# Performance work log

Measured on AMD Instinct MI355X. Metric: run time of the kernel, lower is better.

## Reference

```python
import jax, jax.numpy as jnp
import numpy as np

H_DIM = 1152
N_HEADS = 12
HEAD_DIM = H_DIM // N_HEADS  # 96, divisible by 3
SCALE_ROT = 32 // 16  # character_pixel_size // patch_size


def setup_inputs() -> dict:
    key = jax.random.key(0)
    ks = jax.random.split(key, 9)
    std = 1.0 / np.sqrt(H_DIM)
    return {
        "hidden_states": jax.random.normal(ks[0], (8, 1025, H_DIM), dtype=jnp.float32),
        "Wq": jax.random.normal(ks[1], (H_DIM, H_DIM), dtype=jnp.float32) * std,
        "bq": jax.random.normal(ks[2], (H_DIM,), dtype=jnp.float32) * 0.02,
        "Wk": jax.random.normal(ks[3], (H_DIM, H_DIM), dtype=jnp.float32) * std,
        "bk": jax.random.normal(ks[4], (H_DIM,), dtype=jnp.float32) * 0.02,
        "Wv": jax.random.normal(ks[5], (H_DIM, H_DIM), dtype=jnp.float32) * std,
        "bv": jax.random.normal(ks[6], (H_DIM,), dtype=jnp.float32) * 0.02,
        "Wo": jax.random.normal(ks[7], (H_DIM, H_DIM), dtype=jnp.float32) * std,
        "bo": jax.random.normal(ks[8], (H_DIM,), dtype=jnp.float32) * 0.02,
        "rows": 32,
        "cols": 32,
    }


def _rotary_tables(seq_len, rows, cols, dtype):
    # (seq_len, n_triplets) trig tables based on 2-D patch grid position
    inv_freq = 1.0 / (10000.0 ** (jnp.arange(0, HEAD_DIM, 3, dtype=dtype) / (HEAD_DIM * SCALE_ROT)))
    ids = jnp.arange(seq_len)
    cls_offset = 1 if seq_len != rows * cols else 0
    grid_ids = jnp.clip(ids - cls_offset, 0)
    row_ids = (grid_ids // cols).astype(dtype)
    col_ids = (grid_ids % cols).astype(dtype)
    theta = row_ids[:, None] * inv_freq
    psi = col_ids[:, None] * inv_freq
    return jnp.cos(theta), jnp.sin(theta), jnp.cos(psi), jnp.sin(psi)


def _apply_rotary_3d(x, ct, st, cp, sp):
    # x: (b, s, h, d) -> view as (b, s, h, t, 3)
    b, s, h, d = x.shape
    x = x.reshape(b, s, h, d // 3, 3)
    ct = ct[None, :, None, :]
    st = st[None, :, None, :]
    cp = cp[None, :, None, :]
    sp = sp[None, :, None, :]
    x0, x1, x2 = x[..., 0], x[..., 1], x[..., 2]
    r0 = cp * x0 + sp * st * x1 + sp * ct * x2
    r1 = ct * x1 - st * x2
    r2 = -sp * x0 + cp * st * x1 + cp * ct * x2
    return jnp.stack((r0, r1, r2), axis=-1).reshape(b, s, h, d)


def reference(hidden_states, Wq, bq, Wk, bk, Wv, bv, Wo, bo, rows, cols):
    b, s, _ = hidden_states.shape
    dtype = hidden_states.dtype
    scale = HEAD_DIM ** -0.5

    q = (hidden_states @ Wq + bq).reshape(b, s, N_HEADS, HEAD_DIM)
    k = (hidden_states @ Wk + bk).reshape(b, s, N_HEADS, HEAD_DIM)
    v = (hidden_states @ Wv + bv).reshape(b, s, N_HEADS, HEAD_DIM)

    ct, st, cp, sp = _rotary_tables(s, rows, cols, dtype)
    q = _apply_rotary_3d(q, ct, st, cp, sp)
    k = _apply_rotary_3d(k, ct, st, cp, sp)

    # (b, h, s, s) attention scores
    scores = jnp.einsum("bqhd,bkhd->bhqk", q, k) * scale
    probs = jax.nn.softmax(scores.astype(jnp.float32), axis=-1).astype(dtype)
    ctx = jnp.einsum("bhqk,bkhd->bqhd", probs, v).reshape(b, s, H_DIM)
    out = ctx @ Wo + bo
    return out
```

## Files before the change

### kernel.cpp

```cpp
#include <hip/hip_runtime.h>
#include <stdint.h>

#define BATCH 8
#define SEQ   1025
#define HDIM  1152
#define NH    12
#define DH    96
#define MROWS (BATCH*SEQ)
#define N_QKV (3*HDIM)
#define KD    HDIM
#define NTK   36

typedef __attribute__((ext_vector_type(8))) short short8;
typedef __attribute__((ext_vector_type(4))) short short4_;
typedef __attribute__((ext_vector_type(4))) float float4_;
typedef __attribute__((ext_vector_type(16))) float f32x16;

#define AS1 __attribute__((address_space(1)))
#define AS3 __attribute__((address_space(3)))
#define BARM() do { asm volatile("" ::: "memory"); __builtin_amdgcn_s_barrier(); asm volatile("" ::: "memory"); } while (0)

__device__ inline float bf2f(short s) {
  union { unsigned u; float f; } x; x.u = ((unsigned)(unsigned short)s) << 16; return x.f;
}
__device__ inline short f2bf(float f) {
  union { float f; unsigned u; } x; x.f = f;
  unsigned r = (x.u + 0x7fffu + ((x.u >> 16) & 1u)) >> 16;
  return (short)r;
}

__global__ __launch_bounds__(256) void convx(const float* __restrict__ hs, short* __restrict__ X) {
  int i = blockIdx.x * 256 + threadIdx.x;
  float4_ v = ((const float4_*)hs)[i];
  short4_ o;
  o[0] = f2bf(v[0]); o[1] = f2bf(v[1]); o[2] = f2bf(v[2]); o[3] = f2bf(v[3]);
  ((short4_*)X)[i] = o;
}

__global__ __launch_bounds__(256) void convw_qkv(const float* __restrict__ Wq,
                                                 const float* __restrict__ Wk,
                                                 const float* __restrict__ Wv,
                                                 short* __restrict__ Wt) {
  long e = (long)blockIdx.x * 256 + threadIdx.x;
  int n = (int)(e / KD), k = (int)(e % KD);
  const float* W = n < HDIM ? Wq : (n < 2 * HDIM ? Wk : Wv);
  int nn = n < HDIM ? n : (n < 2 * HDIM ? n - HDIM : n - 2 * HDIM);
  Wt[e] = f2bf(W[(long)k * HDIM + nn]);
}

__global__ __launch_bounds__(256) void convw_o(const float* __restrict__ Wo, short* __restrict__ Wot) {
  long e = (long)blockIdx.x * 256 + threadIdx.x;
  int n = (int)(e / HDIM), k = (int)(e % HDIM);
  Wot[e] = f2bf(Wo[(long)k * HDIM + n]);
}

template<int OUTF32>
__global__ __launch_bounds__(512, 1) void gemm256(
    const short* __restrict__ A, const short* __restrict__ Bt,
    const float* __restrict__ b0, const float* __restrict__ b1, const float* __restrict__ b2,
    void* __restrict__ Cout, const int N, const int MT) {
  __shared__ alignas(16) short Lds[32768];
  const int tid = threadIdx.x;
  const int l = tid & 63, w = tid >> 6;
  const int col = l & 31, hi = l >> 5;
  const int wr = w >> 2, wc = w & 3;

  const int nwg = gridDim.x;
  const int qq = nwg >> 3, r8 = nwg & 7;
  const int xcd = blockIdx.x & 7, loc = blockIdx.x >> 3;
  const int wg = (xcd < r8 ? xcd * (qq + 1) : r8 * (qq + 1) + (xcd - r8) * qq) + loc;
  const int mt = wg % MT, nt = wg / MT;
  const int m0 = mt * 256, n0 = nt * 256;

  const int key = (tid >> 3) & 7;
  const short* asrc[2]; const short* bsrc[2];
#pragma unroll
  for (int i = 0; i < 2; ++i) {
    int g = (i * 512 + tid) ^ key;
    int rowl = g >> 2, colE = (g & 3) * 8;
    int ra = m0 + rowl; if (ra > MROWS - 1) ra = MROWS - 1;
    int rb = n0 + rowl; if (rb > N - 1) rb = N - 1;
    asrc[i] = A + (long)ra * KD + colE;
    bsrc[i] = Bt + (long)rb * KD + colE;
  }

#define STAGE_A(buf, kt_, i) \
  __builtin_amdgcn_global_load_lds((const AS1 void*)(asrc[i] + (kt_) * 32), \
      (AS3 void*)(&Lds[(buf) * 8192 + (i) * 4096 + tid * 8]), 16, 0, 0)
#define STAGE_B(buf, kt_, i) \
  __builtin_amdgcn_global_load_lds((const AS1 void*)(bsrc[i] + (kt_) * 32), \
      (AS3 void*)(&Lds[16384 + (buf) * 8192 + (i) * 4096 + tid * 8]), 16, 0, 0)

  const int keyx = ((col >> 1) & 7) << 3;
  const int fcol = hi * 8;
#define LDSA(buf, mi, ks) (*(const short8*)&Lds[(buf) * 8192 + \
    ((((wr * 128 + (mi) * 32 + col) << 5) + ((ks) << 4) + fcol) ^ keyx)])
#define LDSB(buf, nj, ks) (*(const short8*)&Lds[16384 + (buf) * 8192 + \
    ((((wc * 64 + (nj) * 32 + col) << 5) + ((ks) << 4) + fcol) ^ keyx)])
#define MFMA32(a, b, c) __builtin_amdgcn_mfma_f32_32x32x16_bf16(a, b, c, 0, 0, 0)

  f32x16 acc[4][2];
#pragma unroll
  for (int mi = 0; mi < 4; ++mi)
#pragma unroll
    for (int nj = 0; nj < 2; ++nj) acc[mi][nj] = (f32x16)(0.f);

  STAGE_A(0, 0, 0); STAGE_A(0, 0, 1);
  STAGE_B(0, 0, 0); STAGE_B(0, 0, 1);
  STAGE_B(1, 1, 0); STAGE_B(1, 1, 1);
  asm volatile("s_waitcnt vmcnt(2)" ::: "memory");
  BARM();

  for (int kt = 0; kt < NTK; ++kt) {
    const int cur = kt & 1, nxt = cur ^ 1;
    short8 b00 = LDSB(cur, 0, 0), b01 = LDSB(cur, 0, 1);
    short8 b10 = LDSB(cur, 1, 0), b11 = LDSB(cur, 1, 1);
    short8 a00 = LDSA(cur, 0, 0), a01 = LDSA(cur, 0, 1);
    short8 a10 = LDSA(cur, 1, 0), a11 = LDSA(cur, 1, 1);
    if (kt + 1 < NTK) { STAGE_A(nxt, kt + 1, 0); STAGE_A(nxt, kt + 1, 1); }
    BARM();
    __builtin_amdgcn_s_setprio(1);
    acc[0][0] = MFMA32(a00, b00, acc[0][0]);
    acc[0][1] = MFMA32(a00, b10, acc[0][1]);
    acc[1][0] = MFMA32(a10, b00, acc[1][0]);
    acc[1][1] = MFMA32(a10, b10, acc[1][1]);
    acc[0][0] = MFMA32(a01, b01, acc[0][0]);
    acc[0][1] = MFMA32(a01, b11, acc[0][1]);
    acc[1][0] = MFMA32(a11, b01, acc[1][0]);
    acc[1][1] = MFMA32(a11, b11, acc[1][1]);
    __builtin_amdgcn_s_setprio(0);
    BARM();
    short8 a20 = LDSA(cur, 2, 0), a21 = LDSA(cur, 2, 1);
    short8 a30 = LDSA(cur, 3, 0), a31 = LDSA(cur, 3, 1);
    if (kt + 2 < NTK) { STAGE_B(cur, kt + 2, 0); STAGE_B(cur, kt + 2, 1); }
    if (kt < NTK - 2) asm volatile("s_waitcnt vmcnt(2)" ::: "memory");
    else              asm volatile("s_waitcnt vmcnt(0)" ::: "memory");
    BARM();
    __builtin_amdgcn_s_setprio(1);
    acc[2][0] = MFMA32(a20, b00, acc[2][0]);
    acc[2][1] = MFMA32(a20, b10, acc[2][1]);
    acc[3][0] = MFMA32(a30, b00, acc[3][0]);
    acc[3][1] = MFMA32(a30, b10, acc[3][1]);
    acc[2][0] = MFMA32(a21, b01, acc[2][0]);
    acc[2][1] = MFMA32(a21, b11, acc[2][1]);
    acc[3][0] = MFMA32(a31, b01, acc[3][0]);
    acc[3][1] = MFMA32(a31, b11, acc[3][1]);
    __builtin_amdgcn_s_setprio(0);
    BARM();
  }

  float bias[2];
#pragma unroll
  for (int nj = 0; nj < 2; ++nj) {
    int cn = n0 + wc * 64 + nj * 32 + col;
    float bv_ = 0.f;
    if (cn < N) bv_ = (N == HDIM) ? b0[cn]
                                  : (cn < HDIM ? b0[cn] : (cn < 2 * HDIM ? b1[cn - HDIM] : b2[cn - 2 * HDIM]));
    bias[nj] = bv_;
  }
#pragma unroll
  for (int mi = 0; mi < 4; ++mi)
#pragma unroll
    for (int g = 0; g < 4; ++g)
#pragma unroll
      for (int t2 = 0; t2 < 4; ++t2) {
        int rowi = m0 + wr * 128 + mi * 32 + g * 8 + hi * 4 + t2;
        if (rowi >= MROWS) continue;
#pragma unroll
        for (int nj = 0; nj < 2; ++nj) {
          int cn = n0 + wc * 64 + nj * 32 + col;
          if (cn >= N) continue;
          float v = acc[mi][nj][g * 4 + t2] + bias[nj];
          if (OUTF32) ((float*)Cout)[(long)rowi * N + cn] = v;
          else        ((short*)Cout)[(long)rowi * N + cn] = f2bf(v);
        }
      }
#undef STAGE_A
#undef STAGE_B
#undef LDSA
#undef LDSB
#undef MFMA32
}

__global__ __launch_bounds__(256) void rotary_kernel(short* __restrict__ QKV,
                                                     const int* __restrict__ rowsp,
                                                     const int* __restrict__ colsp) {
  int idx = blockIdx.x * 256 + threadIdx.x;
  int j = idx & 31;
  int t = idx >> 5;
  int h = t % NH;
  int m = t / NH;
  int s = m % SEQ;
  int cols = colsp[0];
  int rws = rowsp[0];
  int off = (SEQ != rws * cols) ? 1 : 0;
  int gid = s - off; if (gid < 0) gid = 0;
  int row = gid / cols, col = gid % cols;
  float invf = exp2f((float)(3 * j) * (-13.287712379549449f / 192.0f));
  float th = row * invf, ps = col * invf;
  float st, ct, sp, cp;
  __sincosf(th, &st, &ct);
  __sincosf(ps, &sp, &cp);
  short* qp = QKV + (long)m * N_QKV + h * DH + 3 * j;
#pragma unroll
  for (int qk = 0; qk < 2; ++qk) {
    short* p = qp + qk * HDIM;
    float x0 = bf2f(p[0]), x1 = bf2f(p[1]), x2 = bf2f(p[2]);
    float r0 =  cp * x0 + sp * st * x1 + sp * ct * x2;
    float r1 =  ct * x1 - st * x2;
    float r2 = -sp * x0 + cp * st * x1 + cp * ct * x2;
    p[0] = f2bf(r0); p[1] = f2bf(r1); p[2] = f2bf(r2);
  }
}

__global__ __launch_bounds__(256) void fragpack(const short* __restrict__ QKV,
                                                short* __restrict__ Kf,
                                                short* __restrict__ Vf) {
  __shared__ short L[64 * 96];
  const int t = blockIdx.x, bh = blockIdx.y;
  const int b = bh / NH, h = bh % NH;
  const int tid = threadIdx.x;
#pragma unroll
  for (int i = 0; i < 3; ++i) {
    int cc = i * 256 + tid;
    int kv = cc / 384;
    int rm = cc % 384;
    int r = rm / 12, m = rm % 12;
    int s = t * 32 + r; if (s > SEQ - 1) s = SEQ - 1;
    const short* src = QKV + (long)(b * SEQ + s) * N_QKV + (kv ? 2 * HDIM : HDIM) + h * DH + m * 8;
    *(short8*)&L[cc * 8] = *(const short8*)src;
  }
  __syncthreads();
#pragma unroll
  for (int i = 0; i < 3; ++i) {
    int oc = i * 256 + tid;
    if (oc < 384) {
      int c = oc / 64, ll = oc & 63;
      int qi = ll & 31, hi = ll >> 5;
      short8 v = *(const short8*)&L[qi * 96 + c * 16 + hi * 8];
      *(short8*)(Kf + (((long)(bh * 33 + t) * 6 + c) * 64 + ll) * 8) = v;
    } else {
      int oc2 = oc - 384;
      int d = oc2 / 128, sl = (oc2 / 64) & 1, ll = oc2 & 63;
      int qi = ll & 31, hi = ll >> 5;
      short8 v;
#pragma unroll
      for (int j = 0; j < 8; ++j)
        v[j] = L[32 * 96 + (sl * 16 + hi * 8 + j) * 96 + d * 32 + qi];
      *(short8*)(Vf + ((((long)(bh * 33 + t) * 3 + d) * 2 + sl) * 64 + ll) * 8) = v;
    }
  }
}

__global__ __launch_bounds__(128, 3) void attn_kernel(const short* __restrict__ QKV,
                                                      const short* __restrict__ Kf,
                                                      const short* __restrict__ Vf,
                                                      short* __restrict__ CTX) {
  const int tid = threadIdx.x;
  const int l = tid & 63, w = tid >> 6;
  const int qi = l & 31, hi = l >> 5;
  const int bid = blockIdx.x;
  const int xcd = bid & 7, jj = bid >> 3;
  const int bh = xcd * 12 + jj / 17;
  const int qb = jj % 17;
  const int b = bh / NH, h = bh % NH;
  const int s = qb * 64 + w * 32 + qi;
  const int sq = s > SEQ - 1 ? SEQ - 1 : s;

  const float scale = 0.1020620726159658f;
  const short* Qr = QKV + (long)(b * SEQ + sq) * N_QKV + h * DH;
  short8 qf[6];
#pragma unroll
  for (int c = 0; c < 6; ++c) {
    short8 v = *(const short8*)(Qr + c * 16 + hi * 8);
#pragma unroll
    for (int j = 0; j < 8; ++j) v[j] = f2bf(bf2f(v[j]) * scale);
    qf[c] = v;
  }

  const short* Kb = Kf + (long)bh * 33 * 6 * 64 * 8;
  const short* Vb = Vf + (long)bh * 33 * 6 * 64 * 8;

  f32x16 ctxv[3];
#pragma unroll
  for (int d = 0; d < 3; ++d) ctxv[d] = (f32x16)(0.f);
  float m_ = -1e30f, l_ = 0.f;

  for (int t = 0; t < 33; ++t) {
    f32x16 S = (f32x16)(0.f);
#pragma unroll
    for (int c = 0; c < 6; ++c) {
      short8 kf = *(const short8*)(Kb + (((long)t * 6 + c) * 64 + l) * 8);
      S = __builtin_amdgcn_mfma_f32_32x32x16_bf16(kf, qf[c], S, 0, 0, 0);
    }
    if (t == 32) {
      S[0] = hi ? -1e30f : S[0];
#pragma unroll
      for (int r = 1; r < 16; ++r) S[r] = -1e30f;
    }
    float tm = S[0];
#pragma unroll
    for (int r = 1; r < 16; ++r) tm = fmaxf(tm, S[r]);
    tm = fmaxf(tm, __shfl_xor(tm, 32));
    if (!__all(tm - m_ <= 8.f)) {
      float mn = fmaxf(m_, tm);
      float alpha = __expf(m_ - mn);
      m_ = mn;
      l_ *= alpha;
#pragma unroll
      for (int d = 0; d < 3; ++d)
#pragma unroll
        for (int r = 0; r < 16; ++r) ctxv[d][r] *= alpha;
    }
    float ts = 0.f;
#pragma unroll
    for (int r = 0; r < 16; ++r) { float p = __expf(S[r] - m_); S[r] = p; ts += p; }
    ts += __shfl_xor(ts, 32);
    l_ += ts;

    unsigned pk_[8];
#pragma unroll
    for (int j = 0; j < 8; ++j)
      pk_[j] = (unsigned)(unsigned short)f2bf(S[2 * j]) |
               ((unsigned)(unsigned short)f2bf(S[2 * j + 1]) << 16);
    unsigned s0 = hi ? pk_[0] : pk_[2];
    unsigned s1 = hi ? pk_[1] : pk_[3];
    unsigned s2 = hi ? pk_[4] : pk_[6];
    unsigned s3 = hi ? pk_[5] : pk_[7];
    unsigned r0 = __shfl_xor(s0, 32);
    unsigned r1 = __shfl_xor(s1, 32);
    unsigned r2 = __shfl_xor(s2, 32);
    unsigned r3 = __shfl_xor(s3, 32);
    union PF { unsigned u[4]; short8 s8; } f0, f1;
    f0.u[0] = hi ? r0 : pk_[0];
    f0.u[1] = hi ? r1 : pk_[1];
    f0.u[2] = hi ? pk_[2] : r0;
    f0.u[3] = hi ? pk_[3] : r1;
    f1.u[0] = hi ? r2 : pk_[4];
    f1.u[1] = hi ? r3 : pk_[5];
    f1.u[2] = hi ? pk_[6] : r2;
    f1.u[3] = hi ? pk_[7] : r3;

#pragma unroll
    for (int d = 0; d < 3; ++d) {
      const short* Vr = Vb + (((long)t * 3 + d) * 2 * 64) * 8;
      short8 vf0 = *(const short8*)(Vr + l * 8);
      ctxv[d] = __builtin_amdgcn_mfma_f32_32x32x16_bf16(vf0, f0.s8, ctxv[d], 0, 0, 0);
      short8 vf1 = *(const short8*)(Vr + (64 + l) * 8);
      ctxv[d] = __builtin_amdgcn_mfma_f32_32x32x16_bf16(vf1, f1.s8, ctxv[d], 0, 0, 0);
    }
  }

  float invl = 1.f / l_;
  if (s <= SEQ - 1) {
    short* Cr = CTX + (long)(b * SEQ + s) * HDIM + h * DH;
#pragma unroll
    for (int d = 0; d < 3; ++d)
#pragma unroll
      for (int g = 0; g < 4; ++g) {
        short4_ o;
#pragma unroll
        for (int r = 0; r < 4; ++r) o[r] = f2bf(ctxv[d][4 * g + r] * invl);
        *(short4_*)(Cr + d * 32 + 8 * g + 4 * hi) = o;
      }
  }
}

extern "C" void kernel_launch(void* const* d_in, const int* in_sizes, int n_in,
                              void* d_out, int out_size, void* d_ws, size_t ws_size,
                              hipStream_t stream) {
  const float* hs = (const float*)d_in[0];
  const float* Wq = (const float*)d_in[1];
  const float* bq = (const float*)d_in[2];
  const float* Wk = (const float*)d_in[3];
  const float* bk = (const float*)d_in[4];
  const float* Wv = (const float*)d_in[5];
  const float* bv = (const float*)d_in[6];
  const float* Wo = (const float*)d_in[7];
  const float* bo = (const float*)d_in[8];
  const int* rows = (const int*)d_in[9];
  const int* cols = (const int*)d_in[10];
  float* out = (float*)d_out;

  char* ws = (char*)d_ws;
  short* X   = (short*)(ws);
  short* Wt  = (short*)(ws + 18892800);
  short* Wot = (short*)(ws + 26855424);
  short* QKV = (short*)(ws + 29509632);
  short* Vf  = (short*)(ws + 86188032);
  short* CTX = (short*)(ws + 105652224);
  short* Kf  = (short*)(ws);

  convx<<<9225, 256, 0, stream>>>(hs, X);
  convw_qkv<<<15552, 256, 0, stream>>>(Wq, Wk, Wv, Wt);
  convw_o<<<5184, 256, 0, stream>>>(Wo, Wot);
  gemm256<0><<<462, 512, 0, stream>>>(X, Wt, bq, bk, bv, QKV, N_QKV, 33);
  rotary_kernel<<<12300, 256, 0, stream>>>(QKV, rows, cols);
  fragpack<<<dim3(33, 96), 256, 0, stream>>>(QKV, Kf, Vf);
  attn_kernel<<<1632, 128, 0, stream>>>(QKV, Kf, Vf, CTX);
  gemm256<1><<<165, 512, 0, stream>>>(CTX, Wot, bo, bo, bo, out, HDIM, 33);
}
```

Measured before the change: 317.5 us.

## Tile weight transposes, triple-buffer GEMM with 16x16 MFMA, fuse K rotary into fragpack

Replaces the strided per-element weight conversion kernels with a shared-memory tiled transpose that reads coalesced float4 and writes 16-byte vectors. The GEMM moves from 32x32 to 16x16x32 bf16 MFMA tiles, uses a new LDS swizzle and a three-stage load buffer prefetching two k-steps ahead. Rotary for Q is now vectorized per thread over 8 triplets, while K rotary is applied inside fragpack in LDS, removing a separate global read/write pass over K. These changes add LDS usage and register pressure in the GEMM and duplicate trig work across blocks.

```diff
diff --git a/kernel.cpp b/kernel.cpp
--- a/kernel.cpp
+++ b/kernel.cpp
@@ -37,21 +37,30 @@
   ((short4_*)X)[i] = o;
 }
 
-__global__ __launch_bounds__(256) void convw_qkv(const float* __restrict__ Wq,
-                                                 const float* __restrict__ Wk,
-                                                 const float* __restrict__ Wv,
-                                                 short* __restrict__ Wt) {
-  long e = (long)blockIdx.x * 256 + threadIdx.x;
-  int n = (int)(e / KD), k = (int)(e % KD);
-  const float* W = n < HDIM ? Wq : (n < 2 * HDIM ? Wk : Wv);
-  int nn = n < HDIM ? n : (n < 2 * HDIM ? n - HDIM : n - 2 * HDIM);
-  Wt[e] = f2bf(W[(long)k * HDIM + nn]);
-}
-
-__global__ __launch_bounds__(256) void convw_o(const float* __restrict__ Wo, short* __restrict__ Wot) {
-  long e = (long)blockIdx.x * 256 + threadIdx.x;
-  int n = (int)(e / HDIM), k = (int)(e % HDIM);
-  Wot[e] = f2bf(Wo[(long)k * HDIM + n]);
+__global__ __launch_bounds__(256) void convw_t(const float* __restrict__ W0,
+                                               const float* __restrict__ W1,
+                                               const float* __restrict__ W2,
+                                               short* __restrict__ Wt) {
+  __shared__ float T[64][65];
+  const int z = blockIdx.z;
+  const float* W = z == 0 ? W0 : (z == 1 ? W1 : W2);
+  const int n0 = blockIdx.x * 64, k0 = blockIdx.y * 64;
+  const int tid = threadIdx.x;
+  const int r = tid >> 2, cq = (tid & 3) * 16;
+#pragma unroll
+  for (int u = 0; u < 4; ++u) {
+    float4_ v = *(const float4_*)&W[(long)(k0 + r) * HDIM + n0 + cq + u * 4];
+    T[r][cq + u * 4 + 0] = v[0]; T[r][cq + u * 4 + 1] = v[1];
+    T[r][cq + u * 4 + 2] = v[2]; T[r][cq + u * 4 + 3] = v[3];
+  }
+  __syncthreads();
+  const int n = tid >> 2, kq = (tid & 3) * 16;
+  short out[16];
+#pragma unroll
+  for (int u = 0; u < 16; ++u) out[u] = f2bf(T[kq + u][n]);
+  short* dst = Wt + (long)(z * HDIM + n0 + n) * KD + k0 + kq;
+  *(short8*)dst = *(short8*)&out[0];
+  *(short8*)(dst + 8) = *(short8*)&out[8];
 }
 
 template<int OUTF32>
@@ -59,10 +68,10 @@
     const short* __restrict__ A, const short* __restrict__ Bt,
     const float* __restrict__ b0, const float* __restrict__ b1, const float* __restrict__ b2,
     void* __restrict__ Cout, const int N, const int MT) {
-  __shared__ alignas(16) short Lds[32768];
+  __shared__ alignas(16) short Lds[49152];
   const int tid = threadIdx.x;
   const int l = tid & 63, w = tid >> 6;
-  const int col = l & 31, hi = l >> 5;
+  const int lrow = l & 15, lg = l >> 4;
   const int wr = w >> 2, wc = w & 3;
 
   const int nwg = gridDim.x;
@@ -72,150 +81,174 @@
   const int mt = wg % MT, nt = wg / MT;
   const int m0 = mt * 256, n0 = nt * 256;
 
-  const int key = (tid >> 3) & 7;
   const short* asrc[2]; const short* bsrc[2];
 #pragma unroll
   for (int i = 0; i < 2; ++i) {
-    int g = (i * 512 + tid) ^ key;
-    int rowl = g >> 2, colE = (g & 3) * 8;
-    int ra = m0 + rowl; if (ra > MROWS - 1) ra = MROWS - 1;
-    int rb = n0 + rowl; if (rb > N - 1) rb = N - 1;
-    asrc[i] = A + (long)ra * KD + colE;
-    bsrc[i] = Bt + (long)rb * KD + colE;
-  }
-
-#define STAGE_A(buf, kt_, i) \
+    int p = i * 512 + tid;
+    int wl = (p & 7) ^ ((p >> 3) & 7);
+    int row = ((p >> 3) << 1) | (wl >> 2);
+    int kc = (wl & 3) * 8;
+    int ra = m0 + row; if (ra > MROWS - 1) ra = MROWS - 1;
+    int rb = n0 + row; if (rb > N - 1) rb = N - 1;
+    asrc[i] = A + (long)ra * KD + kc;
+    bsrc[i] = Bt + (long)rb * KD + kc;
+  }
+
+#define STAGEA(bi, kt_, i) \
   __builtin_amdgcn_global_load_lds((const AS1 void*)(asrc[i] + (kt_) * 32), \
-      (AS3 void*)(&Lds[(buf) * 8192 + (i) * 4096 + tid * 8]), 16, 0, 0)
-#define STAGE_B(buf, kt_, i) \
+      (AS3 void*)(&Lds[(bi) * 8192 + (i * 512 + tid) * 8]), 16, 0, 0)
+#define STAGEB(bi, kt_, i) \
   __builtin_amdgcn_global_load_lds((const AS1 void*)(bsrc[i] + (kt_) * 32), \
-      (AS3 void*)(&Lds[16384 + (buf) * 8192 + (i) * 4096 + tid * 8]), 16, 0, 0)
-
-  const int keyx = ((col >> 1) & 7) << 3;
-  const int fcol = hi * 8;
-#define LDSA(buf, mi, ks) (*(const short8*)&Lds[(buf) * 8192 + \
-    ((((wr * 128 + (mi) * 32 + col) << 5) + ((ks) << 4) + fcol) ^ keyx)])
-#define LDSB(buf, nj, ks) (*(const short8*)&Lds[16384 + (buf) * 8192 + \
-    ((((wc * 64 + (nj) * 32 + col) << 5) + ((ks) << 4) + fcol) ^ keyx)])
-#define MFMA32(a, b, c) __builtin_amdgcn_mfma_f32_32x32x16_bf16(a, b, c, 0, 0, 0)
-
-  f32x16 acc[4][2];
-#pragma unroll
-  for (int mi = 0; mi < 4; ++mi)
-#pragma unroll
-    for (int nj = 0; nj < 2; ++nj) acc[mi][nj] = (f32x16)(0.f);
-
-  STAGE_A(0, 0, 0); STAGE_A(0, 0, 1);
-  STAGE_B(0, 0, 0); STAGE_B(0, 0, 1);
-  STAGE_B(1, 1, 0); STAGE_B(1, 1, 1);
-  asm volatile("s_waitcnt vmcnt(2)" ::: "memory");
+      (AS3 void*)(&Lds[24576 + (bi) * 8192 + (i * 512 + tid) * 8]), 16, 0, 0)
+#define LDA(dst, abase, mi) { const int row_ = wr * 128 + (mi) * 16 + lrow; \
+  dst = *(const short8*)&Lds[(abase) + ((row_ >> 1) << 6) + \
+      (((((row_ & 1) << 2) + lg) ^ ((row_ >> 1) & 7)) << 3)]; }
+#define LDB(dst, bbase, nj) { const int row_ = wc * 64 + (nj) * 16 + lrow; \
+  dst = *(const short8*)&Lds[(bbase) + ((row_ >> 1) << 6) + \
+      (((((row_ & 1) << 2) + lg) ^ ((row_ >> 1) & 7)) << 3)]; }
+#define MFMA16(a, b, c) __builtin_amdgcn_mfma_f32_16x16x32_bf16(a, b, c, 0, 0, 0)
+
+  float4_ acc[8][4];
+#pragma unroll
+  for (int mi = 0; mi < 8; ++mi)
+#pragma unroll
+    for (int nj = 0; nj < 4; ++nj) acc[mi][nj] = (float4_)(0.f);
+
+  STAGEA(0, 0, 0); STAGEA(0, 0, 1); STAGEB(0, 0, 0); STAGEB(0, 0, 1);
+  STAGEA(1, 1, 0); STAGEA(1, 1, 1); STAGEB(1, 1, 0); STAGEB(1, 1, 1);
+  asm volatile("s_waitcnt vmcnt(4)" ::: "memory");
   BARM();
 
+  int cur = 0, st = 2;
   for (int kt = 0; kt < NTK; ++kt) {
-    const int cur = kt & 1, nxt = cur ^ 1;
-    short8 b00 = LDSB(cur, 0, 0), b01 = LDSB(cur, 0, 1);
-    short8 b10 = LDSB(cur, 1, 0), b11 = LDSB(cur, 1, 1);
-    short8 a00 = LDSA(cur, 0, 0), a01 = LDSA(cur, 0, 1);
-    short8 a10 = LDSA(cur, 1, 0), a11 = LDSA(cur, 1, 1);
-    if (kt + 1 < NTK) { STAGE_A(nxt, kt + 1, 0); STAGE_A(nxt, kt + 1, 1); }
+    const bool dost = (kt + 2) < NTK;
+    const int abase = cur * 8192, bbase = 24576 + cur * 8192;
+    short8 a0, a1, a2, a3, bb0, bb1, bb2, bb3;
+    LDA(a0, abase, 0); LDA(a1, abase, 1); LDA(a2, abase, 2); LDA(a3, abase, 3);
+    LDB(bb0, bbase, 0); LDB(bb1, bbase, 1); LDB(bb2, bbase, 2); LDB(bb3, bbase, 3);
+    if (dost) { STAGEA(st, kt + 2, 0); STAGEA(st, kt + 2, 1); }
     BARM();
+    asm volatile("s_waitcnt lgkmcnt(0)" ::: "memory");
+    __builtin_amdgcn_sched_barrier(0);
     __builtin_amdgcn_s_setprio(1);
-    acc[0][0] = MFMA32(a00, b00, acc[0][0]);
-    acc[0][1] = MFMA32(a00, b10, acc[0][1]);
-    acc[1][0] = MFMA32(a10, b00, acc[1][0]);
-    acc[1][1] = MFMA32(a10, b10, acc[1][1]);
-    acc[0][0] = MFMA32(a01, b01, acc[0][0]);
-    acc[0][1] = MFMA32(a01, b11, acc[0][1]);
-    acc[1][0] = MFMA32(a11, b01, acc[1][0]);
-    acc[1][1] = MFMA32(a11, b11, acc[1][1]);
+    acc[0][0] = MFMA16(a0, bb0, acc[0][0]);
+    acc[0][1] = MFMA16(a0, bb1, acc[0][1]);
+    acc[0][2] = MFMA16(a0, bb2, acc[0][2]);
+    acc[0][3] = MFMA16(a0, bb3, acc[0][3]);
+    acc[1][0] = MFMA16(a1, bb0, acc[1][0]);
+    acc[1][1] = MFMA16(a1, bb1, acc[1][1]);
+    acc[1][2] = MFMA16(a1, bb2, acc[1][2]);
+    acc[1][3] = MFMA16(a1, bb3, acc[1][3]);
+    acc[2][0] = MFMA16(a2, bb0, acc[2][0]);
+    acc[2][1] = MFMA16(a2, bb1, acc[2][1]);
+    acc[2][2] = MFMA16(a2, bb2, acc[2][2]);
+    acc[2][3] = MFMA16(a2, bb3, acc[2][3]);
+    acc[3][0] = MFMA16(a3, bb0, acc[3][0]);
+    acc[3][1] = MFMA16(a3, bb1, acc[3][1]);
+    acc[3][2] = MFMA16(a3, bb2, acc[3][2]);
+    acc[3][3] = MFMA16(a3, bb3, acc[3][3]);
     __builtin_amdgcn_s_setprio(0);
     BARM();
-    short8 a20 = LDSA(cur, 2, 0), a21 = LDSA(cur, 2, 1);
-    short8 a30 = LDSA(cur, 3, 0), a31 = LDSA(cur, 3, 1);
-    if (kt + 2 < NTK) { STAGE_B(cur, kt + 2, 0); STAGE_B(cur, kt + 2, 1); }
-    if (kt < NTK - 2) asm volatile("s_waitcnt vmcnt(2)" ::: "memory");
-    else              asm volatile("s_waitcnt vmcnt(0)" ::: "memory");
+    LDA(a0, abase, 4); LDA(a1, abase, 5); LDA(a2, abase, 6); LDA(a3, abase, 7);
+    if (dost) {
+      STAGEB(st, kt + 2, 0); STAGEB(st, kt + 2, 1);
+      asm volatile("s_waitcnt vmcnt(4)" ::: "memory");
+    } else if (kt + 1 < NTK) {
+      asm volatile("s_waitcnt vmcnt(0)" ::: "memory");
+    }
     BARM();
+    asm volatile("s_waitcnt lgkmcnt(0)" ::: "memory");
+    __builtin_amdgcn_sched_barrier(0);
     __builtin_amdgcn_s_setprio(1);
-    acc[2][0] = MFMA32(a20, b00, acc[2][0]);
-    acc[2][1] = MFMA32(a20, b10, acc[2][1]);
-    acc[3][0] = MFMA32(a30, b00, acc[3][0]);
-    acc[3][1] = MFMA32(a30, b10, acc[3][1]);
-    acc[2][0] = MFMA32(a21, b01, acc[2][0]);
-    acc[2][1] = MFMA32(a21, b11, acc[2][1]);
-    acc[3][0] = MFMA32(a31, b01, acc[3][0]);
-    acc[3][1] = MFMA32(a31, b11, acc[3][1]);
+    acc[4][0] = MFMA16(a0, bb0, acc[4][0]);
+    acc[4][1] = MFMA16(a0, bb1, acc[4][1]);
+    acc[4][2] = MFMA16(a0, bb2, acc[4][2]);
+    acc[4][3] = MFMA16(a0, bb3, acc[4][3]);
+    acc[5][0] = MFMA16(a1, bb0, acc[5][0]);
+    acc[5][1] = MFMA16(a1, bb1, acc[5][1]);
+    acc[5][2] = MFMA16(a1, bb2, acc[5][2]);
+    acc[5][3] = MFMA16(a1, bb3, acc[5][3]);
+    acc[6][0] = MFMA16(a2, bb0, acc[6][0]);
+    acc[6][1] = MFMA16(a2, bb1, acc[6][1]);
+    acc[6][2] = MFMA16(a2, bb2, acc[6][2]);
+    acc[6][3] = MFMA16(a2, bb3, acc[6][3]);
+    acc[7][0] = MFMA16(a3, bb0, acc[7][0]);
+    acc[7][1] = MFMA16(a3, bb1, acc[7][1]);
+    acc[7][2] = MFMA16(a3, bb2, acc[7][2]);
+    acc[7][3] = MFMA16(a3, bb3, acc[7][3]);
     __builtin_amdgcn_s_setprio(0);
     BARM();
-  }
-
-  float bias[2];
-#pragma unroll
-  for (int nj = 0; nj < 2; ++nj) {
-    int cn = n0 + wc * 64 + nj * 32 + col;
+    cur = cur == 2 ? 0 : cur + 1;
+    st = st == 2 ? 0 : st + 1;
+  }
+
+  float bias[4];
+#pragma unroll
+  for (int nj = 0; nj < 4; ++nj) {
+    int cn = n0 + wc * 64 + nj * 16 + lrow;
     float bv_ = 0.f;
     if (cn < N) bv_ = (N == HDIM) ? b0[cn]
                                   : (cn < HDIM ? b0[cn] : (cn < 2 * HDIM ? b1[cn - HDIM] : b2[cn - 2 * HDIM]));
     bias[nj] = bv_;
   }
 #pragma unroll
-  for (int mi = 0; mi < 4; ++mi)
-#pragma unroll
-    for (int g = 0; g < 4; ++g)
-#pragma unroll
-      for (int t2 = 0; t2 < 4; ++t2) {
-        int rowi = m0 + wr * 128 + mi * 32 + g * 8 + hi * 4 + t2;
-        if (rowi >= MROWS) continue;
-#pragma unroll
-        for (int nj = 0; nj < 2; ++nj) {
-          int cn = n0 + wc * 64 + nj * 32 + col;
-          if (cn >= N) continue;
-          float v = acc[mi][nj][g * 4 + t2] + bias[nj];
-          if (OUTF32) ((float*)Cout)[(long)rowi * N + cn] = v;
-          else        ((short*)Cout)[(long)rowi * N + cn] = f2bf(v);
-        }
+  for (int mi = 0; mi < 8; ++mi)
+#pragma unroll
+    for (int r = 0; r < 4; ++r) {
+      int m = m0 + wr * 128 + mi * 16 + lg * 4 + r;
+      if (m >= MROWS) continue;
+#pragma unroll
+      for (int nj = 0; nj < 4; ++nj) {
+        int cn = n0 + wc * 64 + nj * 16 + lrow;
+        if (cn >= N) continue;
+        float v = acc[mi][nj][r] + bias[nj];
+        if (OUTF32) ((float*)Cout)[(long)m * N + cn] = v;
+        else        ((short*)Cout)[(long)m * N + cn] = f2bf(v);
       }
-#undef STAGE_A
-#undef STAGE_B
-#undef LDSA
-#undef LDSB
-#undef MFMA32
-}
-
-__global__ __launch_bounds__(256) void rotary_kernel(short* __restrict__ QKV,
-                                                     const int* __restrict__ rowsp,
-                                                     const int* __restrict__ colsp) {
+    }
+#undef STAGEA
+#undef STAGEB
+#undef LDA
+#undef LDB
+#undef MFMA16
+}
+
+__global__ __launch_bounds__(256) void rotary_q(short* __restrict__ QKV,
+                                                const int* __restrict__ rowsp,
+                                                const int* __restrict__ colsp) {
   int idx = blockIdx.x * 256 + threadIdx.x;
-  int j = idx & 31;
-  int t = idx >> 5;
-  int h = t % NH;
-  int m = t / NH;
-  int s = m % SEQ;
-  int cols = colsp[0];
-  int rws = rowsp[0];
-  int off = (SEQ != rws * cols) ? 1 : 0;
+  if (idx >= MROWS * NH * 4) return;
+  const int qt = idx & 3;
+  const int hm = idx >> 2;
+  const int h = hm % NH, m = hm / NH;
+  const int s = m % SEQ;
+  const int cols = colsp[0], rws = rowsp[0];
+  const int off = (SEQ != rws * cols) ? 1 : 0;
   int gid = s - off; if (gid < 0) gid = 0;
-  int row = gid / cols, col = gid % cols;
-  float invf = exp2f((float)(3 * j) * (-13.287712379549449f / 192.0f));
-  float th = row * invf, ps = col * invf;
-  float st, ct, sp, cp;
-  __sincosf(th, &st, &ct);
-  __sincosf(ps, &sp, &cp);
-  short* qp = QKV + (long)m * N_QKV + h * DH + 3 * j;
-#pragma unroll
-  for (int qk = 0; qk < 2; ++qk) {
-    short* p = qp + qk * HDIM;
-    float x0 = bf2f(p[0]), x1 = bf2f(p[1]), x2 = bf2f(p[2]);
-    float r0 =  cp * x0 + sp * st * x1 + sp * ct * x2;
-    float r1 =  ct * x1 - st * x2;
-    float r2 = -sp * x0 + cp * st * x1 + cp * ct * x2;
-    p[0] = f2bf(r0); p[1] = f2bf(r1); p[2] = f2bf(r2);
-  }
+  const float frow = (float)(gid / cols), fcol = (float)(gid % cols);
+  union { short sh[24]; short8 v[3]; } u;
+  short* p = QKV + (long)m * N_QKV + h * DH + qt * 24;
+  u.v[0] = *(short8*)p; u.v[1] = *(short8*)(p + 8); u.v[2] = *(short8*)(p + 16);
+#pragma unroll
+  for (int t = 0; t < 8; ++t) {
+    int j = qt * 8 + t;
+    float invf = exp2f((float)(3 * j) * (-13.287712379549449f / 192.0f));
+    float st, ct, sp, cp;
+    __sincosf(frow * invf, &st, &ct);
+    __sincosf(fcol * invf, &sp, &cp);
+    float x0 = bf2f(u.sh[3 * t]), x1 = bf2f(u.sh[3 * t + 1]), x2 = bf2f(u.sh[3 * t + 2]);
+    u.sh[3 * t]     = f2bf( cp * x0 + sp * st * x1 + sp * ct * x2);
+    u.sh[3 * t + 1] = f2bf( ct * x1 - st * x2);
+    u.sh[3 * t + 2] = f2bf(-sp * x0 + cp * st * x1 + cp * ct * x2);
+  }
+  *(short8*)p = u.v[0]; *(short8*)(p + 8) = u.v[1]; *(short8*)(p + 16) = u.v[2];
 }
 
 __global__ __launch_bounds__(256) void fragpack(const short* __restrict__ QKV,
                                                 short* __restrict__ Kf,
-                                                short* __restrict__ Vf) {
+                                                short* __restrict__ Vf,
+                                                const int* __restrict__ rowsp,
+                                                const int* __restrict__ colsp) {
   __shared__ short L[64 * 96];
   const int t = blockIdx.x, bh = blockIdx.y;
   const int b = bh / NH, h = bh % NH;
@@ -229,6 +262,27 @@
     int s = t * 32 + r; if (s > SEQ - 1) s = SEQ - 1;
     const short* src = QKV + (long)(b * SEQ + s) * N_QKV + (kv ? 2 * HDIM : HDIM) + h * DH + m * 8;
     *(short8*)&L[cc * 8] = *(const short8*)src;
+  }
+  __syncthreads();
+  {
+    const int cols = colsp[0], rws = rowsp[0];
+    const int off = (SEQ != rws * cols) ? 1 : 0;
+#pragma unroll
+    for (int i = 0; i < 4; ++i) {
+      int idx2 = i * 256 + tid;
+      int r = idx2 >> 5, j = idx2 & 31;
+      int s = t * 32 + r; if (s > SEQ - 1) s = SEQ - 1;
+      int gid = s - off; if (gid < 0) gid = 0;
+      float invf = exp2f((float)(3 * j) * (-13.287712379549449f / 192.0f));
+      float st, ct, sp, cp;
+      __sincosf((float)(gid / cols) * invf, &st, &ct);
+      __sincosf((float)(gid % cols) * invf, &sp, &cp);
+      short* pp = &L[r * 96 + 3 * j];
+      float x0 = bf2f(pp[0]), x1 = bf2f(pp[1]), x2 = bf2f(pp[2]);
+      pp[0] = f2bf( cp * x0 + sp * st * x1 + sp * ct * x2);
+      pp[1] = f2bf( ct * x1 - st * x2);
+      pp[2] = f2bf(-sp * x0 + cp * st * x1 + cp * ct * x2);
+    }
   }
   __syncthreads();
 #pragma unroll
@@ -392,11 +446,11 @@
   short* Kf  = (short*)(ws);
 
   convx<<<9225, 256, 0, stream>>>(hs, X);
-  convw_qkv<<<15552, 256, 0, stream>>>(Wq, Wk, Wv, Wt);
-  convw_o<<<5184, 256, 0, stream>>>(Wo, Wot);
+  convw_t<<<dim3(18, 18, 3), 256, 0, stream>>>(Wq, Wk, Wv, Wt);
+  convw_t<<<dim3(18, 18, 1), 256, 0, stream>>>(Wo, Wo, Wo, Wot);
   gemm256<0><<<462, 512, 0, stream>>>(X, Wt, bq, bk, bv, QKV, N_QKV, 33);
-  rotary_kernel<<<12300, 256, 0, stream>>>(QKV, rows, cols);
-  fragpack<<<dim3(33, 96), 256, 0, stream>>>(QKV, Kf, Vf);
+  rotary_q<<<1538, 256, 0, stream>>>(QKV, rows, cols);
+  fragpack<<<dim3(33, 96), 256, 0, stream>>>(QKV, Kf, Vf, rows, cols);
   attn_kernel<<<1632, 128, 0, stream>>>(QKV, Kf, Vf, CTX);
   gemm256<1><<<165, 512, 0, stream>>>(CTX, Wot, bo, bo, bo, out, HDIM, 33);
 }
```

Result: faster. 280.3 us (-11.7%).
